# Kernel optimization log

Measured on AMD Instinct MI355X. Metric: run time of the kernel, lower is better.

The kernel has to match this reference:

```python
import jax, jax.numpy as jnp
from jax import lax
import numpy as np

# Straight-through sign binarization: torch code swaps .data, so autograd
# sees identity through the binarize (STE). Forward value is sign(x).
@jax.custom_vjp
def binarize(x):
    return jnp.sign(x)

def _bin_fwd(x):
    return jnp.sign(x), None

def _bin_bwd(_, g):
    return (g,)

binarize.defvjp(_bin_fwd, _bin_bwd)

EPS = 1e-5

def conv2d(x, w):
    return lax.conv_general_dilated(x, w, (1, 1), 'VALID',
                                    dimension_numbers=('NCHW', 'OIHW', 'NCHW'))

def maxpool2(x):
    return lax.reduce_window(x, -jnp.inf, lax.max, (1, 1, 2, 2), (1, 1, 2, 2), 'VALID')

def bn4(x, g, b, m, v):
    s = g / jnp.sqrt(v + EPS)
    return x * s[None, :, None, None] + (b - m * s)[None, :, None, None]

def bn2(x, g, b, m, v):
    s = g / jnp.sqrt(v + EPS)
    return x * s[None, :] + (b - m * s)[None, :]

def hardtanh(x):
    return jnp.clip(x, -1.0, 1.0)


def setup_inputs() -> dict:
    key = jax.random.key(0)
    ks = jax.random.split(key, 32)
    f32 = jnp.float32
    d = {}
    d['x'] = jax.random.normal(ks[0], (4096, 1, 32, 32), dtype=f32)
    # conv1: 1 -> 18, 5x5
    d['w1'] = jax.random.normal(ks[1], (18, 1, 5, 5), f32) * 0.1
    d['cb1'] = jax.random.normal(ks[2], (18,), f32) * 0.1
    d['g1'] = 1.0 + 0.1 * jax.random.normal(ks[3], (18,), f32)
    d['be1'] = 0.1 * jax.random.normal(ks[4], (18,), f32)
    d['m1'] = 0.1 * jax.random.normal(ks[5], (18,), f32)
    d['v1'] = 0.5 + jax.random.uniform(ks[6], (18,), f32)
    # conv2: 18 -> 48, 5x5
    d['w2'] = jax.random.normal(ks[7], (48, 18, 5, 5), f32) * 0.05
    d['cb2'] = jax.random.normal(ks[8], (48,), f32) * 0.1
    d['g2'] = 1.0 + 0.1 * jax.random.normal(ks[9], (48,), f32)
    d['be2'] = 0.1 * jax.random.normal(ks[10], (48,), f32)
    d['m2'] = 0.1 * jax.random.normal(ks[11], (48,), f32)
    d['v2'] = 0.5 + jax.random.uniform(ks[12], (48,), f32)
    # conv3: 48 -> 120, 5x5
    d['w3'] = jax.random.normal(ks[13], (120, 48, 5, 5), f32) * 0.03
    d['cb3'] = jax.random.normal(ks[14], (120,), f32) * 0.1
    d['g3'] = 1.0 + 0.1 * jax.random.normal(ks[15], (120,), f32)
    d['be3'] = 0.1 * jax.random.normal(ks[16], (120,), f32)
    d['m3'] = 0.1 * jax.random.normal(ks[17], (120,), f32)
    d['v3'] = 0.5 + jax.random.uniform(ks[18], (120,), f32)
    # fc1: 120 -> 252
    d['fw1'] = jax.random.normal(ks[19], (252, 120), f32) * 0.1
    d['fb1'] = jax.random.normal(ks[20], (252,), f32) * 0.1
    d['g4'] = 1.0 + 0.1 * jax.random.normal(ks[21], (252,), f32)
    d['be4'] = 0.1 * jax.random.normal(ks[22], (252,), f32)
    d['m4'] = 0.1 * jax.random.normal(ks[23], (252,), f32)
    d['v4'] = 0.5 + jax.random.uniform(ks[24], (252,), f32)
    # fc2: 252 -> 10
    d['fw2'] = jax.random.normal(ks[25], (10, 252), f32) * 0.1
    d['fb2'] = jax.random.normal(ks[26], (10,), f32) * 0.1
    d['g5'] = 1.0 + 0.1 * jax.random.normal(ks[27], (10,), f32)
    d['be5'] = 0.1 * jax.random.normal(ks[28], (10,), f32)
    d['m5'] = 0.1 * jax.random.normal(ks[29], (10,), f32)
    d['v5'] = 0.5 + jax.random.uniform(ks[30], (10,), f32)
    return d


def reference(x, w1, cb1, g1, be1, m1, v1,
              w2, cb2, g2, be2, m2, v2,
              w3, cb3, g3, be3, m3, v3,
              fw1, fb1, g4, be4, m4, v4,
              fw2, fb2, g5, be5, m5, v5):
    # conv1: input has 1 channel (!=3) -> binarized; weights binarized
    h = conv2d(binarize(x), binarize(w1)) + cb1[None, :, None, None]
    h = hardtanh(bn4(maxpool2(h), g1, be1, m1, v1))
    # conv2
    h = conv2d(binarize(h), binarize(w2)) + cb2[None, :, None, None]
    h = hardtanh(bn4(maxpool2(h), g2, be2, m2, v2))
    # conv3 -> [B,120,1,1]
    h = conv2d(binarize(h), binarize(w3)) + cb3[None, :, None, None]
    h = hardtanh(bn4(h, g3, be3, m3, v3))
    h = h.reshape(-1, 120)
    # fc1: input dim 120 != 784 -> binarized
    h = binarize(h) @ binarize(fw1).T + fb1[None, :]
    h = hardtanh(bn2(h, g4, be4, m4, v4))
    # fc2
    h = binarize(h) @ binarize(fw2).T + fb2[None, :]
    h = bn2(h, g5, be5, m5, v5)
    return jax.nn.log_softmax(h, axis=1)
```

## Files before the change

kernel.cpp:

```cpp
#include <hip/hip_runtime.h>
#include <stdint.h>

typedef int v4i  __attribute__((ext_vector_type(4)));
typedef int v16i __attribute__((ext_vector_type(16)));

#define W1P   0
#define INV1  18
#define CFP   20
#define THRW  104
#define INVM  152
#define B2I   160
#define W3P   9952
#define M3P   14752
#define FW1P  14872
#define M4P   15880
#define FW2P  16132

__device__ inline bool negv(int dot, float B, float S, float T) {
  float v = __fadd_rn((float)dot, B);
  v = __fmul_rn(v, S);
  v = __fadd_rn(v, T);
  return v < 0.0f;
}

__device__ inline void scanMT(float B, float S, float T, int tot, int& M, int& inv) {
  bool b0 = negv(tot, B, S, T);
  bool be = negv(-tot, B, S, T);
  if (b0 == be) { M = 0; inv = b0 ? 0 : 1; return; }
  int lo = 0, hi = tot;
  while (hi - lo > 1) {
    int mid = (lo + hi) >> 1;
    if (negv(tot - 2*mid, B, S, T) == b0) lo = mid; else hi = mid;
  }
  M = hi; inv = b0 ? 1 : 0;
}

__device__ inline float bnS(float g, float v) {
  return __fdiv_rn(g, __fsqrt_rn(__fadd_rn(v, 1e-5f)));
}
__device__ inline float bnT(float be, float m, float s) {
  return __fsub_rn(be, __fmul_rn(m, s));
}

__global__ __launch_bounds__(256) void pack_kernel(
    const float* __restrict__ w1, const float* __restrict__ w2, const float* __restrict__ w3,
    const float* __restrict__ fw1, const float* __restrict__ fw2,
    const float* __restrict__ cb1, const float* __restrict__ g1, const float* __restrict__ be1,
    const float* __restrict__ m1, const float* __restrict__ v1,
    const float* __restrict__ cb2, const float* __restrict__ g2, const float* __restrict__ be2,
    const float* __restrict__ m2, const float* __restrict__ v2,
    const float* __restrict__ cb3, const float* __restrict__ g3, const float* __restrict__ be3,
    const float* __restrict__ m3, const float* __restrict__ v3,
    const float* __restrict__ fb1, const float* __restrict__ g4, const float* __restrict__ be4,
    const float* __restrict__ m4, const float* __restrict__ v4,
    const float* __restrict__ fb2, const float* __restrict__ g5, const float* __restrict__ be5,
    const float* __restrict__ m5, const float* __restrict__ v5,
    uint32_t* __restrict__ wsu)
{
  const int tid = blockIdx.x * 256 + threadIdx.x;

  if (tid < 18) {
    int c = tid;
    uint32_t wt = 0;
    for (int ky = 0; ky < 5; ++ky)
      for (int kx = 0; kx < 5; ++kx)
        if (w1[c*25 + ky*5 + kx] < 0.0f) wt |= 1u << (ky*5 + kx);
    float S = bnS(g1[c], v1[c]);
    float B = cb1[c];
    float T = bnT(be1[c], m1[c], S);
    int M, iv; scanMT(B, S, T, 25, M, iv);
    wsu[W1P + c] = wt | ((uint32_t)M << 25);
  } else if (tid == 18) {
    uint32_t mask = 0;
    for (int c = 0; c < 18; ++c) {
      float S = bnS(g1[c], v1[c]);
      float B = cb1[c];
      float T = bnT(be1[c], m1[c], S);
      int M, iv; scanMT(B, S, T, 25, M, iv);
      if (iv) mask |= 1u << c;
    }
    wsu[INV1] = mask;
  } else if (tid >= 20 && tid < 104) {
    int j = tid - 20;
    float outv;
    if (j < 18) outv = cb1[j];
    else if (j < 36) { int c = j - 18; outv = bnS(g1[c], v1[c]); }
    else if (j < 54) { int c = j - 36; float s = bnS(g1[c], v1[c]); outv = bnT(be1[c], m1[c], s); }
    else if (j < 64) { int c = j - 54; outv = fb2[c]; }
    else if (j < 74) { int c = j - 64; outv = bnS(g5[c], v5[c]); }
    else             { int c = j - 74; float s = bnS(g5[c], v5[c]); outv = bnT(be5[c], m5[c], s); }
    wsu[CFP + j] = __float_as_uint(outv);
  } else if (tid >= 128 && tid < 192) {
    int o = tid - 128;
    bool inv = false;
    if (o < 48) {
      float S = bnS(g2[o], v2[o]);
      float B = cb2[o];
      float T = bnT(be2[o], m2[o], S);
      int M, iv; scanMT(B, S, T, 450, M, iv);
      wsu[THRW + o] = (uint32_t)(450 - 2*M);
      inv = (iv != 0);
    }
    unsigned long long bb = __ballot(inv);
    if (o == 0) {
      wsu[INVM]     = (uint32_t)bb;
      wsu[INVM + 1] = (uint32_t)(bb >> 32) & 0xFFFFu;
    }
  } else if (tid >= 256 && tid < 10048) {
    int idx = tid - 256;
    int o = idx / 204, rem = idx - o*204;
    int k4 = rem * 4;
    uint32_t d = 0;
    if (k4 < 800) {
      int tap = k4 >> 5, cb = k4 & 31;
      #pragma unroll
      for (int j = 0; j < 4; ++j) {
        int c = cb + j;
        uint32_t byte = 0;
        if (c < 18) byte = (w2[(o*18 + c)*25 + tap] < 0.0f) ? 0xFFu : 0x01u;
        d |= byte << (8*j);
      }
    }
    wsu[B2I + (idx ^ (((o >> 3) & 1) << 2))] = d;
  } else if (tid >= 10048 && tid < 14848) {
    int idx = tid - 10048;
    int o = idx / 40, wj = idx - o*40;
    uint32_t b = 0;
    if (wj < 25) {
      int p = wj;
      for (int c = 0; c < 32; ++c)
        if (w3[(o*48 + c)*25 + p] < 0.0f) b |= 1u << c;
    } else if (wj < 38) {
      int j = wj - 25;
      int p0 = 2*j, p1 = 2*j + 1;
      for (int q = 0; q < 16; ++q) {
        int c = 32 + q;
        if (w3[(o*48 + c)*25 + p0] < 0.0f) b |= 1u << q;
        if (p1 < 25 && w3[(o*48 + c)*25 + p1] < 0.0f) b |= 1u << (16 + q);
      }
    }
    wsu[W3P + idx] = b;
  } else if (tid >= 14848 && tid < 14968) {
    int o = tid - 14848;
    float S = bnS(g3[o], v3[o]);
    float B = cb3[o];
    float T = bnT(be3[o], m3[o], S);
    int M, iv; scanMT(B, S, T, 1200, M, iv);
    wsu[M3P + o] = (uint32_t)M | ((uint32_t)iv << 11);
  } else if (tid >= 15104 && tid < 16112) {
    int idx = tid - 15104;
    int o = idx >> 2, wi = idx & 3;
    uint32_t b = 0;
    for (int j = 0; j < 32; ++j) {
      int col = wi*32 + j;
      if (col < 120 && fw1[o*120 + col] < 0.0f) b |= 1u << j;
    }
    wsu[FW1P + idx] = b;
  } else if (tid >= 16128 && tid < 16380) {
    int o = tid - 16128;
    float S = bnS(g4[o], v4[o]);
    float B = fb1[o];
    float T = bnT(be4[o], m4[o], S);
    int M, iv; scanMT(B, S, T, 120, M, iv);
    wsu[M4P + o] = (uint32_t)M | ((uint32_t)iv << 7);
  } else if (tid >= 16384 && tid < 16464) {
    int i = tid - 16384;
    int wi = i / 10, o = i - wi*10;
    uint32_t b = 0;
    for (int j = 0; j < 32; ++j) {
      int col = wi*32 + j;
      if (col < 252 && fw2[o*252 + col] < 0.0f) b |= 1u << j;
    }
    wsu[FW2P + i] = b;
  }
}

#define NIMG 2

__global__ __launch_bounds__(512, 6) void lenet_main(
    const float* __restrict__ x, const uint32_t* __restrict__ wsu,
    float* __restrict__ out)
{
  __shared__ __align__(16) uint8_t Blds[48*816];
  __shared__ __align__(16) uint8_t Alds[NIMG][196*32];
  __shared__ uint32_t xng[NIMG][32], xnz[NIMG][32];
  __shared__ __align__(16) uint32_t h2p[NIMG][40];
  __shared__ uint32_t h3s[NIMG][4];
  __shared__ uint32_t h4s[NIMG][8];
  __shared__ int      sthr[48];
  __shared__ uint32_t lut[16];
  __shared__ int      znz[NIMG][4];

  const int t = threadIdx.x;
  const int it = t & 255;
  const int im = t >> 8;
  const int lane = t & 63;
  const int wv = it >> 6;
  const int img = blockIdx.x * NIMG + im;

  uint4 breg[5];
  {
    const uint4* bsrc = (const uint4*)(wsu + B2I);
    #pragma unroll
    for (int i = 0; i < 5; ++i) {
      int idx = t + i*512;
      breg[i] = (idx < 2448) ? bsrc[idx] : make_uint4(0u,0u,0u,0u);
    }
  }

  {
    const float* xim = x + (size_t)img * 1024;
    const int row = it >> 3, k = it & 7;
    const float4 f = ((const float4*)(xim + row*32))[k];
    const uint32_t u0 = __float_as_uint(f.x), u1 = __float_as_uint(f.y),
                   u2 = __float_as_uint(f.z), u3 = __float_as_uint(f.w);
    uint32_t ng4 = (u0>>31) | ((u1>>31)<<1) | ((u2>>31)<<2) | ((u3>>31)<<3);
    uint32_t nz4 = (uint32_t)((u0<<1)!=0u) | ((uint32_t)((u1<<1)!=0u)<<1)
                 | ((uint32_t)((u2<<1)!=0u)<<2) | ((uint32_t)((u3<<1)!=0u)<<3);
    const bool tok = (nz4 == 0xFu);
    uint32_t ng = ng4 << (4*k), nz = nz4 << (4*k);
    ng |= __shfl_xor(ng, 1);  nz |= __shfl_xor(nz, 1);
    ng |= __shfl_xor(ng, 2);  nz |= __shfl_xor(nz, 2);
    ng |= __shfl_xor(ng, 4);  nz |= __shfl_xor(nz, 4);
    if (k == 0) { xng[im][row] = ng; xnz[im][row] = nz; }
    const int wok = __all(tok);
    if (lane == 0) znz[im][wv] = wok;
  }

  if (t < 16) {
    uint32_t v = 0;
    #pragma unroll
    for (int b = 0; b < 4; ++b) v |= (((t >> b) & 1) ? 0xFFu : 0x01u) << (8*b);
    lut[t] = v;
  }
  if (it < 40) h2p[im][it] = 0;
  if (t >= 64 && t < 112) sthr[t - 64] = (int)wsu[THRW + (t - 64)];

  {
    uint4* bdst = (uint4*)Blds;
    #pragma unroll
    for (int i = 0; i < 5; ++i) {
      int idx = t + i*512;
      if (idx < 2448) bdst[idx] = breg[i];
    }
  }
  __syncthreads();

  const bool zer = !(znz[im][0] & znz[im][1] & znz[im][2] & znz[im][3]);
  if (it < 196) {
    const int py = it / 14, px = it - py*14;
    const int x0 = 2*px, y0 = 2*py;
    uint32_t hm = 0;
    if (!zer) {
      const uint32_t a0 = xng[im][y0+0] >> x0, a1 = xng[im][y0+1] >> x0,
                     a2 = xng[im][y0+2] >> x0, a3 = xng[im][y0+3] >> x0,
                     a4 = xng[im][y0+4] >> x0, a5 = xng[im][y0+5] >> x0;
      const uint32_t w00 = (a0&31u) | ((a1&31u)<<5) | ((a2&31u)<<10) | ((a3&31u)<<15) | ((a4&31u)<<20);
      const uint32_t w01 = ((a0>>1)&31u) | (((a1>>1)&31u)<<5) | (((a2>>1)&31u)<<10) | (((a3>>1)&31u)<<15) | (((a4>>1)&31u)<<20);
      const uint32_t w10 = (a1&31u) | ((a2&31u)<<5) | ((a3&31u)<<10) | ((a4&31u)<<15) | ((a5&31u)<<20);
      const uint32_t w11 = ((a1>>1)&31u) | (((a2>>1)&31u)<<5) | (((a3>>1)&31u)<<10) | (((a4>>1)&31u)<<15) | (((a5>>1)&31u)<<20);
      const uint32_t iv1 = wsu[INV1];
      #pragma unroll
      for (int c = 0; c < 18; ++c) {
        const uint32_t wd = wsu[W1P + c];
        const uint32_t wt = wd & 0x1FFFFFFu;
        const int M = (int)(wd >> 25);
        const int mn = min(min(__popc(w00^wt), __popc(w01^wt)),
                           min(__popc(w10^wt), __popc(w11^wt)));
        hm |= (mn >= M) ? (1u << c) : 0u;
      }
      hm ^= iv1;
    } else {
      uint32_t an[6], az[6];
      #pragma unroll
      for (int r6 = 0; r6 < 6; ++r6) { an[r6] = xng[im][y0+r6] >> x0; az[r6] = xnz[im][y0+r6] >> x0; }
      for (int c = 0; c < 18; ++c) {
        const uint32_t wt = wsu[W1P + c] & 0x1FFFFFFu;
        const float B = __uint_as_float(wsu[CFP + c]);
        const float S = __uint_as_float(wsu[CFP + 18 + c]);
        const float T = __uint_as_float(wsu[CFP + 36 + c]);
        int best = -1000;
        #pragma unroll
        for (int dy = 0; dy < 2; ++dy)
          #pragma unroll
          for (int dx = 0; dx < 2; ++dx) {
            int cnt = 0, ng = 0;
            #pragma unroll
            for (int k = 0; k < 5; ++k) {
              const uint32_t nzr = (az[dy+k] >> dx) & 31u;
              const uint32_t sgr = (an[dy+k] >> dx) & 31u;
              const uint32_t wr  = (wt >> (5*k)) & 31u;
              cnt += __popc(nzr);
              ng  += __popc((sgr ^ wr) & nzr);
            }
            const int conv = cnt - 2*ng;
            best = best > conv ? best : conv;
          }
        if (negv(best, B, S, T)) hm |= 1u << c;
      }
    }
    const uint32_t d0 = lut[hm & 15u];
    const uint32_t d1 = lut[(hm >> 4) & 15u];
    const uint32_t d2 = lut[(hm >> 8) & 15u];
    const uint32_t d3 = lut[(hm >> 12) & 15u];
    const uint32_t d4 = lut[(hm >> 16) & 15u] & 0x0000FFFFu;
    const int swz = (it & 1) << 4;
    uint8_t* ap = &Alds[im][it*32];
    *(uint2*)(ap + swz)            = make_uint2(d0, d1);
    *(uint2*)(ap + swz + 8)        = make_uint2(d2, d3);
    *(uint2*)(ap + (swz ^ 16))     = make_uint2(d4, 0u);
    *(uint2*)(ap + (swz ^ 16) + 8) = make_uint2(0u, 0u);
  }
  __syncthreads();

  {
    const int rl = lane & 31, kh = lane >> 5;
    const int q   = (wv << 3) + (rl >> 2);
    const int qc  = q < 24 ? q : 24;
    const int wnd = rl & 3;
    const int py = qc / 5, px = qc - py*5;
    const int Y0 = 2*py + (wnd >> 1), X0 = 2*px + (wnd & 1);
    const uint32_t pbase = (uint32_t)((Y0*14 + X0) * 32);
    const uint32_t aeven = pbase + (uint32_t)(((kh ^ (X0 & 1)) & 1) << 4);
    const uint32_t aodd  = aeven ^ 16u;
    const int oc0 = rl;
    const int oc1 = rl + 32 < 47 ? rl + 32 : 47;
    const uint8_t* bbase0 = Blds + (((uint32_t)(oc0*816 + (kh << 4))) ^ ((uint32_t)((oc0 >> 3) & 1) << 4));
    const uint8_t* bbase1 = Blds + (((uint32_t)(oc1*816 + (kh << 4))) ^ ((uint32_t)((oc1 >> 3) & 1) << 4));

    v16i acc0 = {};
    v16i acc1 = {};
    #pragma unroll
    for (int ks = 0; ks < 25; ++ks) {
      const int ky = ks / 5, kx = ks - (ks/5)*5;
      const uint32_t aoff = (uint32_t)((ky*14 + kx) * 32);
      v4i a  = *(const v4i*)(&Alds[im][((kx & 1) ? aodd : aeven) + aoff]);
      v4i b0 = *(const v4i*)(bbase0 + ks*32);
      v4i b1 = *(const v4i*)(bbase1 + ks*32);
      acc0 = __builtin_amdgcn_mfma_i32_32x32x32_i8(a, b0, acc0, 0, 0, 0);
      acc1 = __builtin_amdgcn_mfma_i32_32x32x32_i8(a, b1, acc1, 0, 0, 0);
    }

    const int D0 = sthr[oc0];
    const int D1 = sthr[oc1];
    const uint32_t ivm0 = wsu[INVM];
    const uint32_t ivm1d = (wsu[INVM + 1] & 0xFFFFu) * 0x10001u;
    #pragma unroll
    for (int g = 0; g < 4; ++g) {
      const int p0 = max(max(acc0[4*g], acc0[4*g+1]), max(acc0[4*g+2], acc0[4*g+3]));
      const int p1 = max(max(acc1[4*g], acc1[4*g+1]), max(acc1[4*g+2], acc1[4*g+3]));
      unsigned long long e0 = __ballot(p0 <= D0);
      unsigned long long e1 = __ballot(p1 <= D1);
      if (lane == 0) {
        const int pool = (wv << 3) + 2*g;
        if (pool < 25) {
          h2p[im][pool] = (uint32_t)e0 ^ ivm0;
          uint32_t hw = ((uint32_t)e1 & 0xFFFFu) | (((uint32_t)(e1 >> 32) & 0xFFFFu) << 16);
          hw ^= ivm1d;
          if (pool + 1 < 25) h2p[im][pool + 1] = (uint32_t)(e0 >> 32) ^ ivm0;
          else hw &= 0xFFFFu;
          h2p[im][25 + (pool >> 1)] = hw;
        }
      }
    }
  }
  __syncthreads();

  {
    bool pred = false;
    if (it < 240) {
      const int o = it >> 1, h = it & 1;
      const uint4* wp = (const uint4*)(wsu + W3P + o*40 + h*20);
      const uint32_t* hv = &h2p[im][h*20];
      int mm = 0;
      #pragma unroll
      for (int qq = 0; qq < 5; ++qq) {
        const uint4 ww = wp[qq];
        mm += __popc(hv[qq*4+0] ^ ww.x) + __popc(hv[qq*4+1] ^ ww.y)
            + __popc(hv[qq*4+2] ^ ww.z) + __popc(hv[qq*4+3] ^ ww.w);
      }
      mm += __shfl_xor(mm, 1);
      const uint32_t mw = wsu[M3P + o];
      pred = (((mm >= (int)(mw & 2047u)) ? 1u : 0u) ^ (mw >> 11)) != 0u;
    }
    unsigned long long bb = __ballot(pred && ((it & 1) == 0));
    unsigned long long xq = bb & 0x5555555555555555ull;
    xq = (xq | (xq >> 1))  & 0x3333333333333333ull;
    xq = (xq | (xq >> 2))  & 0x0F0F0F0F0F0F0F0Full;
    xq = (xq | (xq >> 4))  & 0x00FF00FF00FF00FFull;
    xq = (xq | (xq >> 8))  & 0x0000FFFF0000FFFFull;
    xq = (xq | (xq >> 16)) & 0x00000000FFFFFFFFull;
    if (lane == 0) h3s[im][wv] = (uint32_t)xq;
  }
  __syncthreads();

  {
    bool pred = false;
    if (it < 252) {
      const uint4 fr = ((const uint4*)(wsu + FW1P))[it];
      const int mm = __popc(h3s[im][0] ^ fr.x) + __popc(h3s[im][1] ^ fr.y)
                   + __popc(h3s[im][2] ^ fr.z) + __popc(h3s[im][3] ^ fr.w);
      const uint32_t mw = wsu[M4P + it];
      pred = (((mm >= (int)(mw & 127u)) ? 1u : 0u) ^ (mw >> 7)) != 0u;
    }
    unsigned long long bb = __ballot(pred);
    if (lane == 0) {
      h4s[im][wv*2]   = (uint32_t)bb;
      h4s[im][wv*2+1] = (uint32_t)(bb >> 32);
    }
  }
  __syncthreads();

  if (it < 16) {
    float vv = -1e30f;
    if (it < 10) {
      int mm = 0;
      #pragma unroll
      for (int wi = 0; wi < 8; ++wi)
        mm += __popc(h4s[im][wi] ^ wsu[FW2P + wi*10 + it]);
      const int dot = 252 - 2*mm;
      const float B = __uint_as_float(wsu[CFP + 54 + it]);
      const float S = __uint_as_float(wsu[CFP + 64 + it]);
      const float T = __uint_as_float(wsu[CFP + 74 + it]);
      float v = __fadd_rn((float)dot, B);
      v = __fmul_rn(v, S);
      vv = __fadd_rn(v, T);
    }
    float mx = vv;
    #pragma unroll
    for (int d = 1; d < 16; d <<= 1)
      mx = fmaxf(mx, __shfl_xor(mx, d, 16));
    const float sh = __fsub_rn(vv, mx);
    float s = expf(sh);
    #pragma unroll
    for (int d = 1; d < 16; d <<= 1)
      s = __fadd_rn(s, __shfl_xor(s, d, 16));
    if (it < 10)
      out[(size_t)img*10 + it] = __fsub_rn(sh, logf(s));
  }
}

extern "C" void kernel_launch(void* const* d_in, const int* in_sizes, int n_in,
                              void* d_out, int out_size, void* d_ws, size_t ws_size,
                              hipStream_t stream)
{
  const float* x   = (const float*)d_in[0];
  const float* w1  = (const float*)d_in[1];
  const float* cb1 = (const float*)d_in[2];
  const float* g1  = (const float*)d_in[3];
  const float* be1 = (const float*)d_in[4];
  const float* m1  = (const float*)d_in[5];
  const float* v1  = (const float*)d_in[6];
  const float* w2  = (const float*)d_in[7];
  const float* cb2 = (const float*)d_in[8];
  const float* g2  = (const float*)d_in[9];
  const float* be2 = (const float*)d_in[10];
  const float* m2  = (const float*)d_in[11];
  const float* v2  = (const float*)d_in[12];
  const float* w3  = (const float*)d_in[13];
  const float* cb3 = (const float*)d_in[14];
  const float* g3  = (const float*)d_in[15];
  const float* be3 = (const float*)d_in[16];
  const float* m3  = (const float*)d_in[17];
  const float* v3  = (const float*)d_in[18];
  const float* fw1 = (const float*)d_in[19];
  const float* fb1 = (const float*)d_in[20];
  const float* g4  = (const float*)d_in[21];
  const float* be4 = (const float*)d_in[22];
  const float* m4  = (const float*)d_in[23];
  const float* v4  = (const float*)d_in[24];
  const float* fw2 = (const float*)d_in[25];
  const float* fb2 = (const float*)d_in[26];
  const float* g5  = (const float*)d_in[27];
  const float* be5 = (const float*)d_in[28];
  const float* m5  = (const float*)d_in[29];
  const float* v5  = (const float*)d_in[30];

  uint32_t* wsu = (uint32_t*)d_ws;
  float* out = (float*)d_out;

  hipLaunchKernelGGL(pack_kernel, dim3(65), dim3(256), 0, stream,
                     w1, w2, w3, fw1, fw2,
                     cb1, g1, be1, m1, v1,
                     cb2, g2, be2, m2, v2,
                     cb3, g3, be3, m3, v3,
                     fb1, g4, be4, m4, v4,
                     fb2, g5, be5, m5, v5,
                     wsu);

  hipLaunchKernelGGL(lenet_main, dim3(2048), dim3(512), 0, stream,
                     x, wsu, out);
}
```

Baseline: 42.13 us.

## Run conv3, fc1 and fc2 tail in a single wavefront per image without barriers

The tail layers (conv3, fc1, fc2 plus log-softmax) used to be spread across four wavefronts per image and handed results through shared memory, with two block-wide barriers in between. Now wave 0 of each image loads the pooled conv2 bits into registers and computes all 120 conv3 outputs, 252 fc1 outputs and the fc2 logits itself, passing them along with ballots. This drops two __syncthreads and the shared-memory round trips. In exchange the tail runs on fewer lanes, does more serial work per lane and uses more registers, which may lower occupancy.

```diff
diff --git a/kernel.cpp b/kernel.cpp
--- a/kernel.cpp
+++ b/kernel.cpp
@@ -185,8 +185,6 @@
   __shared__ __align__(16) uint8_t Alds[NIMG][196*32];
   __shared__ uint32_t xng[NIMG][32], xnz[NIMG][32];
   __shared__ __align__(16) uint32_t h2p[NIMG][40];
-  __shared__ uint32_t h3s[NIMG][4];
-  __shared__ uint32_t h4s[NIMG][8];
   __shared__ int      sthr[48];
   __shared__ uint32_t lut[16];
   __shared__ int      znz[NIMG][4];
@@ -366,62 +364,63 @@
   }
   __syncthreads();
 
-  {
-    bool pred = false;
-    if (it < 240) {
-      const int o = it >> 1, h = it & 1;
-      const uint4* wp = (const uint4*)(wsu + W3P + o*40 + h*20);
-      const uint32_t* hv = &h2p[im][h*20];
-      int mm = 0;
-      #pragma unroll
-      for (int qq = 0; qq < 5; ++qq) {
-        const uint4 ww = wp[qq];
-        mm += __popc(hv[qq*4+0] ^ ww.x) + __popc(hv[qq*4+1] ^ ww.y)
-            + __popc(hv[qq*4+2] ^ ww.z) + __popc(hv[qq*4+3] ^ ww.w);
-      }
-      mm += __shfl_xor(mm, 1);
-      const uint32_t mw = wsu[M3P + o];
-      pred = (((mm >= (int)(mw & 2047u)) ? 1u : 0u) ^ (mw >> 11)) != 0u;
-    }
-    unsigned long long bb = __ballot(pred && ((it & 1) == 0));
-    unsigned long long xq = bb & 0x5555555555555555ull;
-    xq = (xq | (xq >> 1))  & 0x3333333333333333ull;
-    xq = (xq | (xq >> 2))  & 0x0F0F0F0F0F0F0F0Full;
-    xq = (xq | (xq >> 4))  & 0x00FF00FF00FF00FFull;
-    xq = (xq | (xq >> 8))  & 0x0000FFFF0000FFFFull;
-    xq = (xq | (xq >> 16)) & 0x00000000FFFFFFFFull;
-    if (lane == 0) h3s[im][wv] = (uint32_t)xq;
-  }
-  __syncthreads();
-
-  {
-    bool pred = false;
-    if (it < 252) {
-      const uint4 fr = ((const uint4*)(wsu + FW1P))[it];
-      const int mm = __popc(h3s[im][0] ^ fr.x) + __popc(h3s[im][1] ^ fr.y)
-                   + __popc(h3s[im][2] ^ fr.z) + __popc(h3s[im][3] ^ fr.w);
-      const uint32_t mw = wsu[M4P + it];
-      pred = (((mm >= (int)(mw & 127u)) ? 1u : 0u) ^ (mw >> 7)) != 0u;
-    }
-    unsigned long long bb = __ballot(pred);
-    if (lane == 0) {
-      h4s[im][wv*2]   = (uint32_t)bb;
-      h4s[im][wv*2+1] = (uint32_t)(bb >> 32);
-    }
-  }
-  __syncthreads();
-
-  if (it < 16) {
+  if (wv == 0) {
+    uint32_t h2r[40];
+    #pragma unroll
+    for (int i = 0; i < 10; ++i) {
+      const uint4 v = *(const uint4*)&h2p[im][i*4];
+      h2r[i*4+0] = v.x; h2r[i*4+1] = v.y; h2r[i*4+2] = v.z; h2r[i*4+3] = v.w;
+    }
+
+    uint32_t h3r[4];
+    #pragma unroll
+    for (int r = 0; r < 2; ++r) {
+      const int o = lane + 64*r;
+      bool pred = false;
+      if (o < 120) {
+        const uint4* wp = (const uint4*)(wsu + W3P + o*40);
+        int mm = 0;
+        #pragma unroll
+        for (int qq = 0; qq < 10; ++qq) {
+          const uint4 ww = wp[qq];
+          mm += __popc(h2r[qq*4+0] ^ ww.x) + __popc(h2r[qq*4+1] ^ ww.y)
+              + __popc(h2r[qq*4+2] ^ ww.z) + __popc(h2r[qq*4+3] ^ ww.w);
+        }
+        const uint32_t mw = wsu[M3P + o];
+        pred = (((mm >= (int)(mw & 2047u)) ? 1u : 0u) ^ (mw >> 11)) != 0u;
+      }
+      unsigned long long bb = __ballot(pred);
+      h3r[2*r]   = (uint32_t)bb;
+      h3r[2*r+1] = (uint32_t)(bb >> 32);
+    }
+
+    uint32_t h4r[8];
+    #pragma unroll
+    for (int r = 0; r < 4; ++r) {
+      const int o = lane + 64*r;
+      bool pred = false;
+      if (o < 252) {
+        const uint4 fr = ((const uint4*)(wsu + FW1P))[o];
+        const int mm = __popc(h3r[0] ^ fr.x) + __popc(h3r[1] ^ fr.y)
+                     + __popc(h3r[2] ^ fr.z) + __popc(h3r[3] ^ fr.w);
+        const uint32_t mw = wsu[M4P + o];
+        pred = (((mm >= (int)(mw & 127u)) ? 1u : 0u) ^ (mw >> 7)) != 0u;
+      }
+      unsigned long long bb = __ballot(pred);
+      h4r[2*r]   = (uint32_t)bb;
+      h4r[2*r+1] = (uint32_t)(bb >> 32);
+    }
+
     float vv = -1e30f;
-    if (it < 10) {
+    if (lane < 10) {
       int mm = 0;
       #pragma unroll
       for (int wi = 0; wi < 8; ++wi)
-        mm += __popc(h4s[im][wi] ^ wsu[FW2P + wi*10 + it]);
+        mm += __popc(h4r[wi] ^ wsu[FW2P + wi*10 + lane]);
       const int dot = 252 - 2*mm;
-      const float B = __uint_as_float(wsu[CFP + 54 + it]);
-      const float S = __uint_as_float(wsu[CFP + 64 + it]);
-      const float T = __uint_as_float(wsu[CFP + 74 + it]);
+      const float B = __uint_as_float(wsu[CFP + 54 + lane]);
+      const float S = __uint_as_float(wsu[CFP + 64 + lane]);
+      const float T = __uint_as_float(wsu[CFP + 74 + lane]);
       float v = __fadd_rn((float)dot, B);
       v = __fmul_rn(v, S);
       vv = __fadd_rn(v, T);
@@ -435,8 +434,8 @@
     #pragma unroll
     for (int d = 1; d < 16; d <<= 1)
       s = __fadd_rn(s, __shfl_xor(s, d, 16));
-    if (it < 10)
-      out[(size_t)img*10 + it] = __fsub_rn(sh, logf(s));
+    if (lane < 10)
+      out[(size_t)img*10 + lane] = __fsub_rn(sh, logf(s));
   }
 }
 
```

Result: slower. 46.38 us (+10.1%).

## Read conv2 weight fragments directly from global memory instead of staging in LDS

Applied to the files above, without the earlier changes.

The conv2 binarized weights are repacked in the pack kernel into a per-tap, per-output-slot layout padded to 64 slots. The main kernel then loads MFMA B operands straight from global/L2 instead of copying about 39 KB into LDS per block. This drops the per-block staging loads, LDS writes and a large LDS allocation, which may allow more resident blocks. In exchange every wave issues global loads inside the MFMA loop, adding latency and depending on cache hits.

```diff
diff --git a/kernel.cpp b/kernel.cpp
--- a/kernel.cpp
+++ b/kernel.cpp
@@ -10,11 +10,11 @@
 #define THRW  104
 #define INVM  152
 #define B2I   160
-#define W3P   9952
-#define M3P   14752
-#define FW1P  14872
-#define M4P   15880
-#define FW2P  16132
+#define W3P   12960
+#define M3P   17760
+#define FW1P  17880
+#define M4P   18888
+#define FW2P  19140
 
 __device__ inline bool negv(int dot, float B, float S, float T) {
   float v = __fadd_rn((float)dot, B);
@@ -106,24 +106,24 @@
       wsu[INVM]     = (uint32_t)bb;
       wsu[INVM + 1] = (uint32_t)(bb >> 32) & 0xFFFFu;
     }
-  } else if (tid >= 256 && tid < 10048) {
+  } else if (tid >= 256 && tid < 13056) {
     int idx = tid - 256;
-    int o = idx / 204, rem = idx - o*204;
-    int k4 = rem * 4;
+    int ks   = idx >> 9;
+    int slot = (idx >> 3) & 63;
+    int w4   = idx & 7;
     uint32_t d = 0;
-    if (k4 < 800) {
-      int tap = k4 >> 5, cb = k4 & 31;
+    if (slot < 48) {
       #pragma unroll
       for (int j = 0; j < 4; ++j) {
-        int c = cb + j;
+        int c = w4*4 + j;
         uint32_t byte = 0;
-        if (c < 18) byte = (w2[(o*18 + c)*25 + tap] < 0.0f) ? 0xFFu : 0x01u;
+        if (c < 18) byte = (w2[(slot*18 + c)*25 + ks] < 0.0f) ? 0xFFu : 0x01u;
         d |= byte << (8*j);
       }
     }
-    wsu[B2I + (idx ^ (((o >> 3) & 1) << 2))] = d;
-  } else if (tid >= 10048 && tid < 14848) {
-    int idx = tid - 10048;
+    wsu[B2I + idx] = d;
+  } else if (tid >= 13056 && tid < 17856) {
+    int idx = tid - 13056;
     int o = idx / 40, wj = idx - o*40;
     uint32_t b = 0;
     if (wj < 25) {
@@ -140,15 +140,15 @@
       }
     }
     wsu[W3P + idx] = b;
-  } else if (tid >= 14848 && tid < 14968) {
-    int o = tid - 14848;
+  } else if (tid >= 17856 && tid < 17976) {
+    int o = tid - 17856;
     float S = bnS(g3[o], v3[o]);
     float B = cb3[o];
     float T = bnT(be3[o], m3[o], S);
     int M, iv; scanMT(B, S, T, 1200, M, iv);
     wsu[M3P + o] = (uint32_t)M | ((uint32_t)iv << 11);
-  } else if (tid >= 15104 && tid < 16112) {
-    int idx = tid - 15104;
+  } else if (tid >= 17976 && tid < 18984) {
+    int idx = tid - 17976;
     int o = idx >> 2, wi = idx & 3;
     uint32_t b = 0;
     for (int j = 0; j < 32; ++j) {
@@ -156,15 +156,15 @@
       if (col < 120 && fw1[o*120 + col] < 0.0f) b |= 1u << j;
     }
     wsu[FW1P + idx] = b;
-  } else if (tid >= 16128 && tid < 16380) {
-    int o = tid - 16128;
+  } else if (tid >= 18984 && tid < 19236) {
+    int o = tid - 18984;
     float S = bnS(g4[o], v4[o]);
     float B = fb1[o];
     float T = bnT(be4[o], m4[o], S);
     int M, iv; scanMT(B, S, T, 120, M, iv);
     wsu[M4P + o] = (uint32_t)M | ((uint32_t)iv << 7);
-  } else if (tid >= 16384 && tid < 16464) {
-    int i = tid - 16384;
+  } else if (tid >= 19236 && tid < 19316) {
+    int i = tid - 19236;
     int wi = i / 10, o = i - wi*10;
     uint32_t b = 0;
     for (int j = 0; j < 32; ++j) {
@@ -181,7 +181,6 @@
     const float* __restrict__ x, const uint32_t* __restrict__ wsu,
     float* __restrict__ out)
 {
-  __shared__ __align__(16) uint8_t Blds[48*816];
   __shared__ __align__(16) uint8_t Alds[NIMG][196*32];
   __shared__ uint32_t xng[NIMG][32], xnz[NIMG][32];
   __shared__ __align__(16) uint32_t h2p[NIMG][40];
@@ -197,16 +196,6 @@
   const int lane = t & 63;
   const int wv = it >> 6;
   const int img = blockIdx.x * NIMG + im;
-
-  uint4 breg[5];
-  {
-    const uint4* bsrc = (const uint4*)(wsu + B2I);
-    #pragma unroll
-    for (int i = 0; i < 5; ++i) {
-      int idx = t + i*512;
-      breg[i] = (idx < 2448) ? bsrc[idx] : make_uint4(0u,0u,0u,0u);
-    }
-  }
 
   {
     const float* xim = x + (size_t)img * 1024;
@@ -235,15 +224,6 @@
   }
   if (it < 40) h2p[im][it] = 0;
   if (t >= 64 && t < 112) sthr[t - 64] = (int)wsu[THRW + (t - 64)];
-
-  {
-    uint4* bdst = (uint4*)Blds;
-    #pragma unroll
-    for (int i = 0; i < 5; ++i) {
-      int idx = t + i*512;
-      if (idx < 2448) bdst[idx] = breg[i];
-    }
-  }
   __syncthreads();
 
   const bool zer = !(znz[im][0] & znz[im][1] & znz[im][2] & znz[im][3]);
@@ -323,10 +303,7 @@
     const uint32_t pbase = (uint32_t)((Y0*14 + X0) * 32);
     const uint32_t aeven = pbase + (uint32_t)(((kh ^ (X0 & 1)) & 1) << 4);
     const uint32_t aodd  = aeven ^ 16u;
-    const int oc0 = rl;
-    const int oc1 = rl + 32 < 47 ? rl + 32 : 47;
-    const uint8_t* bbase0 = Blds + (((uint32_t)(oc0*816 + (kh << 4))) ^ ((uint32_t)((oc0 >> 3) & 1) << 4));
-    const uint8_t* bbase1 = Blds + (((uint32_t)(oc1*816 + (kh << 4))) ^ ((uint32_t)((oc1 >> 3) & 1) << 4));
+    const uint8_t* bg = (const uint8_t*)(wsu + B2I) + (rl*32 + kh*16);
 
     v16i acc0 = {};
     v16i acc1 = {};
@@ -335,14 +312,14 @@
       const int ky = ks / 5, kx = ks - (ks/5)*5;
       const uint32_t aoff = (uint32_t)((ky*14 + kx) * 32);
       v4i a  = *(const v4i*)(&Alds[im][((kx & 1) ? aodd : aeven) + aoff]);
-      v4i b0 = *(const v4i*)(bbase0 + ks*32);
-      v4i b1 = *(const v4i*)(bbase1 + ks*32);
+      v4i b0 = *(const v4i*)(bg + ks*2048);
+      v4i b1 = *(const v4i*)(bg + ks*2048 + 1024);
       acc0 = __builtin_amdgcn_mfma_i32_32x32x32_i8(a, b0, acc0, 0, 0, 0);
       acc1 = __builtin_amdgcn_mfma_i32_32x32x32_i8(a, b1, acc1, 0, 0, 0);
     }
 
-    const int D0 = sthr[oc0];
-    const int D1 = sthr[oc1];
+    const int D0 = sthr[rl];
+    const int D1 = sthr[rl + 32 < 47 ? rl + 32 : 47];
     const uint32_t ivm0 = wsu[INVM];
     const uint32_t ivm1d = (wsu[INVM + 1] & 0xFFFFu) * 0x10001u;
     #pragma unroll
@@ -479,7 +456,7 @@
   uint32_t* wsu = (uint32_t*)d_ws;
   float* out = (float*)d_out;
 
-  hipLaunchKernelGGL(pack_kernel, dim3(65), dim3(256), 0, stream,
+  hipLaunchKernelGGL(pack_kernel, dim3(76), dim3(256), 0, stream,
                      w1, w2, w3, fw1, fw2,
                      cb1, g1, be1, m1, v1,
                      cb2, g2, be2, m2, v2,
```

Result: slower. 46.74 us (+10.9%).
